# Kernel tuning notes

Hardware: AMD Instinct MI355X
Metric: run time of the kernel (lower is better)

## Reference

```python
import jax, jax.numpy as jnp
import numpy as np

EPS_LN = 1e-5

def _layernorm(x, g, b):
    mu = jnp.mean(x, axis=-1, keepdims=True)
    var = jnp.mean((x - mu) ** 2, axis=-1, keepdims=True)
    return (x - mu) * jax.lax.rsqrt(var + EPS_LN) * g + b

def _act_quant_ste(x):
    # clip_val uses detached stats -> stop_gradient
    clip_val = jax.lax.stop_gradient(
        jnp.clip(jnp.mean(jnp.abs(x), axis=-1, keepdims=True), 1e-8, None)) * 2.5
    scale = clip_val / 127.0
    x_scaled = x / scale
    x_clip = jnp.clip(x_scaled, -127.0, 127.0)
    x_q = x_scaled + jax.lax.stop_gradient(jnp.round(x_clip) - x_scaled)
    return x_q * scale

def _weight_quant_ste(w):
    scale = jax.lax.stop_gradient(jnp.clip(jnp.mean(jnp.abs(w)), 1e-8, None))
    w_norm = w / scale
    w_clip = jnp.clip(w_norm, -1.0, 1.0)
    w_q = w_norm + jax.lax.stop_gradient(jnp.round(w_clip) - w_norm)
    return w_q * scale

def _bitlinear(x, w, g, b):
    # w: [out, in]; x: [B,T,in]
    x_q = _act_quant_ste(_layernorm(x, g, b))
    w_q = _weight_quant_ste(w)
    return jnp.einsum('btd,hd->bth', x_q, w_q)

def setup_inputs() -> dict:
    D, H = 2048, 2048 * 4
    B, T = 4, 2048
    key = jax.random.key(0)
    ks = jax.random.split(key, 4)
    std = 0.02
    return {
        'x': jax.random.normal(ks[0], (B, T, D), dtype=jnp.float32),
        'mu_k': jnp.zeros((1, 1, D), jnp.float32),
        'mu_r': jnp.zeros((1, 1, D), jnp.float32),
        'wk': jax.random.normal(ks[1], (H, D), jnp.float32) * std,
        'gk': jnp.ones((D,), jnp.float32), 'bk': jnp.zeros((D,), jnp.float32),
        'wr': jax.random.normal(ks[2], (D, D), jnp.float32) * std,
        'gr': jnp.ones((D,), jnp.float32), 'br': jnp.zeros((D,), jnp.float32),
        'wv': jax.random.normal(ks[3], (D, H), jnp.float32) * std,
        'gv': jnp.ones((H,), jnp.float32), 'bv': jnp.zeros((H,), jnp.float32),
    }

def reference(x, mu_k, mu_r, wk, gk, bk, wr, gr, br, wv, gv, bv):
    B, T, C = x.shape
    prev = jnp.zeros((B, 1, C), dtype=x.dtype)  # state=None path
    x_prev = jnp.concatenate([prev, x[:, :-1, :]], axis=1)  # token shift
    dx = x_prev - x
    k_act = jax.nn.relu(_bitlinear(x + dx * mu_k, wk, gk, bk)) ** 2  # [B,T,H]
    rgate = jax.nn.sigmoid(_bitlinear(x + dx * mu_r, wr, gr, br))    # [B,T,D]
    out = rgate * _bitlinear(k_act, wv, gv, bv)                      # [B,T,D]
    return out, jax.lax.stop_gradient(x[:, -1:, :])
```

## Files before the change

### kernel.cpp

```cpp
#include <hip/hip_runtime.h>

#define T_LEN 2048
#define B_SZ  4
#define D_DIM 2048
#define H_DIM 8192
#define BT    (B_SZ * T_LEN)

typedef float f32x4 __attribute__((ext_vector_type(4)));
typedef int   i32x4v __attribute__((ext_vector_type(4)));
typedef int   i32x16v __attribute__((ext_vector_type(16)));
typedef unsigned short ushort8 __attribute__((ext_vector_type(8)));

__device__ __forceinline__ float bf2f(unsigned short u) {
    unsigned int i = ((unsigned int)u) << 16;
    return __builtin_bit_cast(float, i);
}
__device__ __forceinline__ unsigned short f2bf(float f) {
    unsigned int i = __builtin_bit_cast(unsigned int, f);
    i += 0x7fffu + ((i >> 16) & 1u);
    return (unsigned short)(i >> 16);
}

__device__ __forceinline__ float block_sum(float v, float* red) {
    #pragma unroll
    for (int o = 32; o > 0; o >>= 1) v += __shfl_down(v, o, 64);
    const int lane = threadIdx.x & 63, w = threadIdx.x >> 6;
    if (lane == 0) red[w] = v;
    __syncthreads();
    float r = red[0] + red[1] + red[2] + red[3];
    __syncthreads();
    return r;
}

__global__ void wabs_all(const float* __restrict__ wk, const float* __restrict__ wr,
                         const float* __restrict__ wv, float* __restrict__ part) {
    __shared__ float red[16];
    const int m = blockIdx.x >> 10;
    const int blk = blockIdx.x & 1023;
    const float* w = (m == 0) ? wk : (m == 1) ? wr : wv;
    const int n = (m == 1) ? D_DIM * D_DIM : H_DIM * D_DIM;
    float s = 0.f;
    int i = (blk * 256 + threadIdx.x) * 8;
    const int stride = 1024 * 256 * 8;
    for (; i < n; i += stride) {
        f32x4 a = *(const f32x4*)(w + i);
        f32x4 b = *(const f32x4*)(w + i + 4);
        #pragma unroll
        for (int j = 0; j < 4; j++) s += fabsf(a[j]) + fabsf(b[j]);
    }
    float tot = block_sum(s, red);
    if (threadIdx.x == 0) part[blockIdx.x] = tot;
}

__global__ void wfinal_all(const float* __restrict__ part, float* __restrict__ wsc) {
    __shared__ float red[16];
    const int m = blockIdx.x;
    const int n = (m == 1) ? D_DIM * D_DIM : H_DIM * D_DIM;
    float s = 0.f;
    for (int i = threadIdx.x; i < 1024; i += 256) s += part[m * 1024 + i];
    float tot = block_sum(s, red);
    if (threadIdx.x == 0) wsc[m] = fmaxf(tot / (float)n, 1e-8f);
}

__global__ void wquant_all(const float* __restrict__ wk, const float* __restrict__ wr,
                           const float* __restrict__ wv,
                           signed char* __restrict__ qk, signed char* __restrict__ qr,
                           signed char* __restrict__ qv,
                           const float* __restrict__ wsc) {
    const int b = blockIdx.x;
    int m, blk, nblk;
    if (b < 2048)      { m = 0; blk = b;        nblk = 2048; }
    else if (b < 3072) { m = 1; blk = b - 2048; nblk = 1024; }
    else               { m = 2; blk = b - 3072; nblk = 2048; }
    const float* w = (m == 0) ? wk : (m == 1) ? wr : wv;
    signed char* q = (m == 0) ? qk : (m == 1) ? qr : qv;
    const int n = (m == 1) ? D_DIM * D_DIM : H_DIM * D_DIM;
    const float s = wsc[m];
    int i = (blk * 256 + threadIdx.x) * 16;
    const int stride = nblk * 256 * 16;
    for (; i < n; i += stride) {
        union { signed char c[16]; i32x4v v; } pk;
        #pragma unroll
        for (int h = 0; h < 4; h++) {
            f32x4 a = *(const f32x4*)(w + i + h * 4);
            #pragma unroll
            for (int j = 0; j < 4; j++)
                pk.c[h * 4 + j] =
                    (signed char)(int)rintf(fminf(fmaxf(a[j] / s, -1.f), 1.f));
        }
        *(i32x4v*)(q + i) = pk.v;
    }
}

__device__ __forceinline__ void ln_quant8(const float* xm_in,
                                          const float* __restrict__ g,
                                          const float* __restrict__ b,
                                          signed char* qrow, float* srow, float* red) {
    const int base = threadIdx.x * 8;
    float xm[8];
    float s = 0.f;
    #pragma unroll
    for (int j = 0; j < 8; j++) { xm[j] = xm_in[j]; s += xm[j]; }
    const float mean = block_sum(s, red) * (1.f / D_DIM);
    float s2 = 0.f;
    #pragma unroll
    for (int j = 0; j < 8; j++) { float d = xm[j] - mean; s2 += d * d; }
    const float var  = block_sum(s2, red) * (1.f / D_DIM);
    const float rstd = 1.f / sqrtf(var + 1e-5f);
    f32x4 ga = *(const f32x4*)(g + base), gb = *(const f32x4*)(g + base + 4);
    f32x4 ba = *(const f32x4*)(b + base), bb2 = *(const f32x4*)(b + base + 4);
    float gg[8] = {ga[0],ga[1],ga[2],ga[3],gb[0],gb[1],gb[2],gb[3]};
    float bb[8] = {ba[0],ba[1],ba[2],ba[3],bb2[0],bb2[1],bb2[2],bb2[3]};
    float sa = 0.f;
    #pragma unroll
    for (int j = 0; j < 8; j++) {
        xm[j] = (xm[j] - mean) * rstd * gg[j] + bb[j];
        sa += fabsf(xm[j]);
    }
    const float amean = block_sum(sa, red) * (1.f / D_DIM);
    const float scale = fmaxf(amean, 1e-8f) * 2.5f / 127.0f;
    union { signed char c[8]; int2 v; } pk;
    #pragma unroll
    for (int j = 0; j < 8; j++)
        pk.c[j] = (signed char)(int)rintf(fminf(fmaxf(xm[j] / scale, -127.f), 127.f));
    *(int2*)(qrow + base) = pk.v;
    if (threadIdx.x == 0) *srow = scale;
}

__global__ void act_prep(const float* __restrict__ x,
                         const float* __restrict__ muk,
                         const float* __restrict__ gk, const float* __restrict__ bk,
                         const float* __restrict__ mur,
                         const float* __restrict__ gr, const float* __restrict__ br,
                         signed char* __restrict__ qk, float* __restrict__ sk,
                         signed char* __restrict__ qr, float* __restrict__ sr,
                         float* __restrict__ out2) {
    __shared__ float red[16];
    const int row = blockIdx.x;
    const int t = row & (T_LEN - 1);
    const int base = threadIdx.x * 8;

    float xv[8], xp[8];
    f32x4 xa = *(const f32x4*)(x + (size_t)row * D_DIM + base);
    f32x4 xb = *(const f32x4*)(x + (size_t)row * D_DIM + base + 4);
    xv[0]=xa[0]; xv[1]=xa[1]; xv[2]=xa[2]; xv[3]=xa[3];
    xv[4]=xb[0]; xv[5]=xb[1]; xv[6]=xb[2]; xv[7]=xb[3];
    if (t > 0) {
        f32x4 pa = *(const f32x4*)(x + (size_t)(row - 1) * D_DIM + base);
        f32x4 pb = *(const f32x4*)(x + (size_t)(row - 1) * D_DIM + base + 4);
        xp[0]=pa[0]; xp[1]=pa[1]; xp[2]=pa[2]; xp[3]=pa[3];
        xp[4]=pb[0]; xp[5]=pb[1]; xp[6]=pb[2]; xp[7]=pb[3];
    } else {
        #pragma unroll
        for (int j = 0; j < 8; j++) xp[j] = 0.f;
    }
    if (t == T_LEN - 1) {
        const int bb = row / T_LEN;
        *(f32x4*)(out2 + (size_t)bb * D_DIM + base)     = xa;
        *(f32x4*)(out2 + (size_t)bb * D_DIM + base + 4) = xb;
    }
    float mk[8], mr[8], xmk[8], xmr[8];
    f32x4 mka = *(const f32x4*)(muk + base), mkb = *(const f32x4*)(muk + base + 4);
    f32x4 mra = *(const f32x4*)(mur + base), mrb = *(const f32x4*)(mur + base + 4);
    mk[0]=mka[0]; mk[1]=mka[1]; mk[2]=mka[2]; mk[3]=mka[3];
    mk[4]=mkb[0]; mk[5]=mkb[1]; mk[6]=mkb[2]; mk[7]=mkb[3];
    mr[0]=mra[0]; mr[1]=mra[1]; mr[2]=mra[2]; mr[3]=mra[3];
    mr[4]=mrb[0]; mr[5]=mrb[1]; mr[6]=mrb[2]; mr[7]=mrb[3];
    #pragma unroll
    for (int j = 0; j < 8; j++) {
        const float dx = xp[j] - xv[j];
        xmk[j] = xv[j] + dx * mk[j];
        xmr[j] = xv[j] + dx * mr[j];
    }
    ln_quant8(xmk, gk, bk, qk + (size_t)row * D_DIM, sk + row, red);
    ln_quant8(xmr, gr, br, qr + (size_t)row * D_DIM, sr + row, red);
}

__global__ void lnq_v(const unsigned short* __restrict__ kact,
                      const float* __restrict__ g, const float* __restrict__ b,
                      signed char* __restrict__ qv, float* __restrict__ sv) {
    __shared__ float red[16];
    const int row = blockIdx.x;
    const int base = threadIdx.x * 32;
    const unsigned short* kr = kact + (size_t)row * H_DIM + base;

    float v[32];
    float s = 0.f;
    #pragma unroll
    for (int c = 0; c < 4; c++) {
        ushort8 a = *(const ushort8*)(kr + c * 8);
        #pragma unroll
        for (int j = 0; j < 8; j++) { v[c * 8 + j] = bf2f(a[j]); s += v[c * 8 + j]; }
    }
    const float mean = block_sum(s, red) * (1.f / H_DIM);
    float s2 = 0.f;
    #pragma unroll
    for (int j = 0; j < 32; j++) { float d = v[j] - mean; s2 += d * d; }
    const float var  = block_sum(s2, red) * (1.f / H_DIM);
    const float rstd = 1.f / sqrtf(var + 1e-5f);
    float sa = 0.f;
    #pragma unroll
    for (int c = 0; c < 8; c++) {
        f32x4 ga = *(const f32x4*)(g + base + c * 4);
        f32x4 ba = *(const f32x4*)(b + base + c * 4);
        #pragma unroll
        for (int j = 0; j < 4; j++) {
            int k = c * 4 + j;
            v[k] = (v[k] - mean) * rstd * ga[j] + ba[j];
            sa += fabsf(v[k]);
        }
    }
    const float amean = block_sum(sa, red) * (1.f / H_DIM);
    const float scale = fmaxf(amean, 1e-8f) * 2.5f / 127.0f;
    union { signed char c[32]; i32x4v v4[2]; } pk;
    #pragma unroll
    for (int j = 0; j < 32; j++)
        pk.c[j] = (signed char)(int)rintf(fminf(fmaxf(v[j] / scale, -127.f), 127.f));
    *(i32x4v*)(qv + (size_t)row * H_DIM + base)      = pk.v4[0];
    *(i32x4v*)(qv + (size_t)row * H_DIM + base + 16) = pk.v4[1];
    if (threadIdx.x == 0) sv[row] = scale;
}

__global__ __launch_bounds__(512, 2) void gemmA(
    const signed char* __restrict__ A, const signed char* __restrict__ B,
    int K, int Nn, int gn,
    const float* __restrict__ sa, const float* __restrict__ swp,
    unsigned short* __restrict__ out_bf) {
    __shared__ signed char Bs[2][128 * 64];
    const int tid = threadIdx.x;
    const int nwg = gridDim.x, q8 = nwg >> 3;
    const int swz = (blockIdx.x & 7) * q8 + (blockIdx.x >> 3);
    const int bm = swz / gn, bn = swz % gn;
    const int lane = tid & 63, wave = tid >> 6;
    const int lrow = lane & 31, lhalf = lane >> 5;
    const size_t arow0 = (size_t)bm * 512;
    const size_t brow0 = (size_t)bn * 128;
    const int NT = K >> 6;

    i32x16v acc[2][4] = {};

    auto stageB = [&](int buf, int k0) {
        const int r = tid >> 2, sl = tid & 3;
        const signed char* g = B + (brow0 + r) * (size_t)K + k0 + ((sl ^ ((r >> 1) & 3)) * 16);
        __builtin_amdgcn_global_load_lds(
            (const __attribute__((address_space(1))) void*)g,
            (__attribute__((address_space(3))) void*)(Bs[buf] + tid * 16), 16, 0, 0);
    };
    auto loadA = [&](i32x4v (&a)[2][2], int k0) {
        #pragma unroll
        for (int tm = 0; tm < 2; tm++)
            #pragma unroll
            for (int s = 0; s < 2; s++) {
                const int r = wave * 64 + tm * 32 + lrow;
                a[tm][s] = *(const i32x4v*)(A + (arow0 + r) * (size_t)K + k0 + (s * 2 + lhalf) * 16);
            }
    };
    auto readB = [&](const signed char* BsB, i32x4v (&b)[4][2]) {
        #pragma unroll
        for (int s = 0; s < 2; s++) {
            const int slot = s * 2 + lhalf;
            #pragma unroll
            for (int tn = 0; tn < 4; tn++) {
                const int r = tn * 32 + lrow;
                b[tn][s] = *(const i32x4v*)(BsB + r * 64 + ((slot ^ ((r >> 1) & 3)) * 16));
            }
        }
    };
    auto mfma8 = [&](i32x4v (&a)[2][2], i32x4v (&b)[4][2]) {
        #pragma unroll
        for (int s = 0; s < 2; s++)
            #pragma unroll
            for (int tm = 0; tm < 2; tm++)
                #pragma unroll
                for (int tn = 0; tn < 4; tn++)
                    acc[tm][tn] = __builtin_amdgcn_mfma_i32_32x32x32_i8(
                        a[tm][s], b[tn][s], acc[tm][tn], 0, 0, 0);
    };

    i32x4v a0[2][2], a1[2][2];
    stageB(0, 0);
    loadA(a0, 0);
    for (int it = 0; it < NT / 2; it++) {
        const int t0 = 2 * it, t1 = t0 + 1;
        stageB(1, t1 << 6);
        loadA(a1, t1 << 6);
        asm volatile("s_waitcnt vmcnt(5)" ::: "memory");
        __builtin_amdgcn_sched_barrier(0);
        __builtin_amdgcn_s_barrier();
        __builtin_amdgcn_sched_barrier(0);
        {
            i32x4v b[4][2];
            readB(Bs[0], b);
            __builtin_amdgcn_s_setprio(1);
            mfma8(a0, b);
            __builtin_amdgcn_s_setprio(0);
        }
        __builtin_amdgcn_sched_barrier(0);
        __builtin_amdgcn_s_barrier();
        if (t1 + 1 < NT) {
            stageB(0, (t1 + 1) << 6);
            loadA(a0, (t1 + 1) << 6);
            asm volatile("s_waitcnt vmcnt(5)" ::: "memory");
        } else {
            asm volatile("s_waitcnt vmcnt(0)" ::: "memory");
        }
        __builtin_amdgcn_sched_barrier(0);
        __builtin_amdgcn_s_barrier();
        __builtin_amdgcn_sched_barrier(0);
        {
            i32x4v b[4][2];
            readB(Bs[1], b);
            __builtin_amdgcn_s_setprio(1);
            mfma8(a1, b);
            __builtin_amdgcn_s_setprio(0);
        }
        __builtin_amdgcn_sched_barrier(0);
        __builtin_amdgcn_s_barrier();
    }

    const float sw = *swp;
    #pragma unroll
    for (int tm = 0; tm < 2; tm++) {
        #pragma unroll
        for (int tn = 0; tn < 4; tn++) {
            #pragma unroll
            for (int rg = 0; rg < 16; rg++) {
                const int rin  = (rg & 3) + 8 * (rg >> 2) + 4 * lhalf;
                const int grow = bm * 512 + wave * 64 + tm * 32 + rin;
                const int gcol = bn * 128 + tn * 32 + lrow;
                const float v = (float)acc[tm][tn][rg] * sa[grow] * sw;
                float rv = fmaxf(v, 0.f);
                out_bf[(size_t)grow * Nn + gcol] = f2bf(rv * rv);
            }
        }
    }
}

template <int EP>
__global__ __launch_bounds__(256) void gemm_i8(
    const signed char* __restrict__ A, const signed char* __restrict__ B,
    int K, int Nn,
    const float* __restrict__ sa, const float* __restrict__ swp,
    const unsigned short* __restrict__ gate_bf, float* __restrict__ out_f,
    unsigned short* __restrict__ out_gbf) {
    __shared__ signed char As[128 * 128];
    __shared__ signed char Bs[128 * 128];
    const int tid  = threadIdx.x;
    const int bm   = blockIdx.x, bn = blockIdx.y;
    const int lane = tid & 63, wave = tid >> 6;
    const int wr = wave >> 1, wc = wave & 1;
    const int lrow = lane & 31, lhalf = lane >> 5;

    i32x16v acc[2][2] = {};

    int srow[4], scol[4];
    #pragma unroll
    for (int i = 0; i < 4; i++) {
        int o = i * 256 + tid;
        int r = o >> 3, sl = o & 7;
        srow[i] = r;
        scol[i] = ((sl ^ (r & 7)) * 16);
    }
    const size_t arow0 = (size_t)bm * 128;
    const size_t brow0 = (size_t)bn * 128;

    for (int k0 = 0; k0 < K; k0 += 128) {
        __syncthreads();
        #pragma unroll
        for (int i = 0; i < 4; i++) {
            const signed char* ga = A + (arow0 + srow[i]) * (size_t)K + k0 + scol[i];
            const signed char* gb = B + (brow0 + srow[i]) * (size_t)K + k0 + scol[i];
            __builtin_amdgcn_global_load_lds(
                (const __attribute__((address_space(1))) void*)ga,
                (__attribute__((address_space(3))) void*)(As + (i * 256 + tid) * 16),
                16, 0, 0);
            __builtin_amdgcn_global_load_lds(
                (const __attribute__((address_space(1))) void*)gb,
                (__attribute__((address_space(3))) void*)(Bs + (i * 256 + tid) * 16),
                16, 0, 0);
        }
        __syncthreads();

        #pragma unroll
        for (int ks = 0; ks < 4; ks++) {
            const int slot = ks * 2 + lhalf;
            i32x4v af[2], bfv[2];
            #pragma unroll
            for (int tm = 0; tm < 2; tm++) {
                int r = wr * 64 + tm * 32 + lrow;
                af[tm] = *(const i32x4v*)(As + r * 128 + ((slot ^ (r & 7)) * 16));
            }
            #pragma unroll
            for (int tn = 0; tn < 2; tn++) {
                int r = wc * 64 + tn * 32 + lrow;
                bfv[tn] = *(const i32x4v*)(Bs + r * 128 + ((slot ^ (r & 7)) * 16));
            }
            #pragma unroll
            for (int tm = 0; tm < 2; tm++)
                #pragma unroll
                for (int tn = 0; tn < 2; tn++)
                    acc[tm][tn] = __builtin_amdgcn_mfma_i32_32x32x32_i8(
                        af[tm], bfv[tn], acc[tm][tn], 0, 0, 0);
        }
    }

    const float sw = *swp;
    #pragma unroll
    for (int tm = 0; tm < 2; tm++) {
        #pragma unroll
        for (int tn = 0; tn < 2; tn++) {
            #pragma unroll
            for (int rg = 0; rg < 16; rg++) {
                const int rin  = (rg & 3) + 8 * (rg >> 2) + 4 * lhalf;
                const int grow = bm * 128 + wr * 64 + tm * 32 + rin;
                const int gcol = bn * 128 + wc * 64 + tn * 32 + lrow;
                const float v = (float)acc[tm][tn][rg] * sa[grow] * sw;
                const size_t idx = (size_t)grow * Nn + gcol;
                if (EP == 1) {
                    out_gbf[idx] = f2bf(1.0f / (1.0f + expf(-v)));
                } else {
                    out_f[idx] = bf2f(gate_bf[idx]) * v;
                }
            }
        }
    }
}

extern "C" void kernel_launch(void* const* d_in, const int* in_sizes, int n_in,
                              void* d_out, int out_size, void* d_ws, size_t ws_size,
                              hipStream_t stream) {
    const float* x   = (const float*)d_in[0];
    const float* muk = (const float*)d_in[1];
    const float* mur = (const float*)d_in[2];
    const float* wk  = (const float*)d_in[3];
    const float* gk  = (const float*)d_in[4];
    const float* bk  = (const float*)d_in[5];
    const float* wr  = (const float*)d_in[6];
    const float* gr  = (const float*)d_in[7];
    const float* br  = (const float*)d_in[8];
    const float* wv  = (const float*)d_in[9];
    const float* gv  = (const float*)d_in[10];
    const float* bv  = (const float*)d_in[11];

    char* wsb = (char*)d_ws;
    size_t off = 0;
    auto alloc = [&](size_t bytes) -> size_t {
        size_t p = off;
        off = (off + bytes + 255) & ~(size_t)255;
        return p;
    };
    const size_t o_wqk  = alloc((size_t)H_DIM * D_DIM);
    const size_t o_wqr  = alloc((size_t)D_DIM * D_DIM);
    const size_t o_wqv  = alloc((size_t)D_DIM * H_DIM);
    const size_t o_wsc  = alloc(64);
    const size_t o_part = alloc(3 * 1024 * sizeof(float));
    const size_t o_xqk  = alloc((size_t)BT * D_DIM);
    const size_t o_xqr  = alloc((size_t)BT * D_DIM);
    const size_t o_gate = alloc((size_t)BT * D_DIM * 2);
    const size_t o_sk   = alloc((size_t)BT * 4);
    const size_t o_sr   = alloc((size_t)BT * 4);
    const size_t fixed  = off;

    int CH = BT;
    while (CH > 512 &&
           fixed + (size_t)CH * (H_DIM + 2 * H_DIM + 4) + 8192 > ws_size)
        CH >>= 1;
    const size_t o_xqv  = alloc((size_t)CH * H_DIM);
    const size_t o_kact = alloc((size_t)CH * H_DIM * 2);
    const size_t o_sv   = alloc((size_t)CH * 4);

    signed char* wqk = (signed char*)(wsb + o_wqk);
    signed char* wqr = (signed char*)(wsb + o_wqr);
    signed char* wqv = (signed char*)(wsb + o_wqv);
    float* wsc  = (float*)(wsb + o_wsc);
    float* part = (float*)(wsb + o_part);
    signed char* xqk = (signed char*)(wsb + o_xqk);
    signed char* xqr = (signed char*)(wsb + o_xqr);
    unsigned short* gate = (unsigned short*)(wsb + o_gate);
    float* sk = (float*)(wsb + o_sk);
    float* sr = (float*)(wsb + o_sr);
    signed char* xqv = (signed char*)(wsb + o_xqv);
    unsigned short* kact = (unsigned short*)(wsb + o_kact);
    float* sv = (float*)(wsb + o_sv);

    float* outp = (float*)d_out;
    float* out2 = outp + (size_t)BT * D_DIM;

    wabs_all<<<3072, 256, 0, stream>>>(wk, wr, wv, part);
    wfinal_all<<<3, 256, 0, stream>>>(part, wsc);
    wquant_all<<<5120, 256, 0, stream>>>(wk, wr, wv, wqk, wqr, wqv, wsc);

    act_prep<<<BT, 256, 0, stream>>>(x, muk, gk, bk, mur, gr, br,
                                     xqk, sk, xqr, sr, out2);

    gemm_i8<1><<<dim3(BT / 128, D_DIM / 128), 256, 0, stream>>>(
        xqr, wqr, D_DIM, D_DIM, sr, wsc + 1,
        (const unsigned short*)nullptr, (float*)nullptr, gate);

    for (int row0 = 0; row0 < BT; row0 += CH) {
        gemmA<<<(CH / 512) * (H_DIM / 128), 512, 0, stream>>>(
            xqk + (size_t)row0 * D_DIM, wqk, D_DIM, H_DIM, H_DIM / 128,
            sk + row0, wsc + 0, kact);

        lnq_v<<<CH, 256, 0, stream>>>(kact, gv, bv, xqv, sv);

        gemm_i8<2><<<dim3(CH / 128, D_DIM / 128), 256, 0, stream>>>(
            xqv, wqv, H_DIM, D_DIM, sv, wsc + 2,
            gate + (size_t)row0 * D_DIM, outp + (size_t)row0 * D_DIM,
            (unsigned short*)nullptr);
    }
}
```

Before: 652.7 us.

## Unify int8 GEMMs into templated register-A kernel with 4-stage B pipeline

Replaces the separate 128x128 LDS-staged gemm_i8 kernel with a templated version of the register-A, LDS-B GEMM. It now runs with 256-row tiles for the r-gate and v projections and 512-row tiles for the k projection. The B buffer grows to four LDS stages with a prefetch distance of two, which leaves one barrier per k-step instead of two. The aim is better latency hiding and less synchronisation on all three GEMMs. In exchange it uses more LDS and larger tiles, which means fewer workgroups for the D-output GEMMs.

```diff
diff --git a/kernel.cpp b/kernel.cpp
--- a/kernel.cpp
+++ b/kernel.cpp
@@ -221,23 +221,26 @@
     if (threadIdx.x == 0) sv[row] = scale;
 }
 
-__global__ __launch_bounds__(512, 2) void gemmA(
+template <int EP, int MT>
+__global__ __launch_bounds__(512, 2) void gemmR(
     const signed char* __restrict__ A, const signed char* __restrict__ B,
     int K, int Nn, int gn,
     const float* __restrict__ sa, const float* __restrict__ swp,
+    const unsigned short* __restrict__ gate_bf, float* __restrict__ out_f,
     unsigned short* __restrict__ out_bf) {
-    __shared__ signed char Bs[2][128 * 64];
+    constexpr int BM = MT * 256;
+    __shared__ signed char Bs[4][128 * 64];
     const int tid = threadIdx.x;
     const int nwg = gridDim.x, q8 = nwg >> 3;
     const int swz = (blockIdx.x & 7) * q8 + (blockIdx.x >> 3);
     const int bm = swz / gn, bn = swz % gn;
     const int lane = tid & 63, wave = tid >> 6;
     const int lrow = lane & 31, lhalf = lane >> 5;
-    const size_t arow0 = (size_t)bm * 512;
+    const size_t arow0 = (size_t)bm * BM;
     const size_t brow0 = (size_t)bn * 128;
     const int NT = K >> 6;
 
-    i32x16v acc[2][4] = {};
+    i32x16v acc[MT][4] = {};
 
     auto stageB = [&](int buf, int k0) {
         const int r = tid >> 2, sl = tid & 3;
@@ -246,12 +249,12 @@
             (const __attribute__((address_space(1))) void*)g,
             (__attribute__((address_space(3))) void*)(Bs[buf] + tid * 16), 16, 0, 0);
     };
-    auto loadA = [&](i32x4v (&a)[2][2], int k0) {
-        #pragma unroll
-        for (int tm = 0; tm < 2; tm++)
+    auto loadA = [&](i32x4v (&a)[MT][2], int k0) {
+        #pragma unroll
+        for (int tm = 0; tm < MT; tm++)
             #pragma unroll
             for (int s = 0; s < 2; s++) {
-                const int r = wave * 64 + tm * 32 + lrow;
+                const int r = wave * (MT * 32) + tm * 32 + lrow;
                 a[tm][s] = *(const i32x4v*)(A + (arow0 + r) * (size_t)K + k0 + (s * 2 + lhalf) * 16);
             }
     };
@@ -266,158 +269,69 @@
             }
         }
     };
-    auto mfma8 = [&](i32x4v (&a)[2][2], i32x4v (&b)[4][2]) {
+    auto mfmaT = [&](i32x4v (&a)[MT][2], i32x4v (&b)[4][2]) {
         #pragma unroll
         for (int s = 0; s < 2; s++)
             #pragma unroll
-            for (int tm = 0; tm < 2; tm++)
+            for (int tm = 0; tm < MT; tm++)
                 #pragma unroll
                 for (int tn = 0; tn < 4; tn++)
                     acc[tm][tn] = __builtin_amdgcn_mfma_i32_32x32x32_i8(
                         a[tm][s], b[tn][s], acc[tm][tn], 0, 0, 0);
     };
 
-    i32x4v a0[2][2], a1[2][2];
+    i32x4v aE[MT][2], aO[MT][2];
     stageB(0, 0);
-    loadA(a0, 0);
-    for (int it = 0; it < NT / 2; it++) {
-        const int t0 = 2 * it, t1 = t0 + 1;
-        stageB(1, t1 << 6);
-        loadA(a1, t1 << 6);
-        asm volatile("s_waitcnt vmcnt(5)" ::: "memory");
+    loadA(aE, 0);
+    stageB(1, 64);
+
+    auto body = [&](int t, i32x4v (&cur)[MT][2], i32x4v (&nxt)[MT][2]) {
+        const bool hasA = (t + 1 < NT);
+        const bool hasB = (t + 2 < NT);
+        if (hasA) loadA(nxt, (t + 1) << 6);
+        if (hasB) stageB((t + 2) & 3, (t + 2) << 6);
+        if (hasB) {
+            if constexpr (MT == 2) asm volatile("s_waitcnt vmcnt(6)" ::: "memory");
+            else                   asm volatile("s_waitcnt vmcnt(4)" ::: "memory");
+        } else if (hasA) {
+            if constexpr (MT == 2) asm volatile("s_waitcnt vmcnt(5)" ::: "memory");
+            else                   asm volatile("s_waitcnt vmcnt(3)" ::: "memory");
+        } else {
+            asm volatile("s_waitcnt vmcnt(0)" ::: "memory");
+        }
         __builtin_amdgcn_sched_barrier(0);
         __builtin_amdgcn_s_barrier();
-        __builtin_amdgcn_sched_barrier(0);
         {
             i32x4v b[4][2];
-            readB(Bs[0], b);
+            readB(Bs[t & 3], b);
             __builtin_amdgcn_s_setprio(1);
-            mfma8(a0, b);
+            mfmaT(cur, b);
             __builtin_amdgcn_s_setprio(0);
         }
-        __builtin_amdgcn_sched_barrier(0);
-        __builtin_amdgcn_s_barrier();
-        if (t1 + 1 < NT) {
-            stageB(0, (t1 + 1) << 6);
-            loadA(a0, (t1 + 1) << 6);
-            asm volatile("s_waitcnt vmcnt(5)" ::: "memory");
-        } else {
-            asm volatile("s_waitcnt vmcnt(0)" ::: "memory");
-        }
-        __builtin_amdgcn_sched_barrier(0);
-        __builtin_amdgcn_s_barrier();
-        __builtin_amdgcn_sched_barrier(0);
-        {
-            i32x4v b[4][2];
-            readB(Bs[1], b);
-            __builtin_amdgcn_s_setprio(1);
-            mfma8(a1, b);
-            __builtin_amdgcn_s_setprio(0);
-        }
-        __builtin_amdgcn_sched_barrier(0);
-        __builtin_amdgcn_s_barrier();
+    };
+
+    for (int t = 0; t < NT; t += 2) {
+        body(t, aE, aO);
+        body(t + 1, aO, aE);
     }
 
     const float sw = *swp;
     #pragma unroll
-    for (int tm = 0; tm < 2; tm++) {
+    for (int tm = 0; tm < MT; tm++) {
         #pragma unroll
         for (int tn = 0; tn < 4; tn++) {
             #pragma unroll
             for (int rg = 0; rg < 16; rg++) {
                 const int rin  = (rg & 3) + 8 * (rg >> 2) + 4 * lhalf;
-                const int grow = bm * 512 + wave * 64 + tm * 32 + rin;
+                const int grow = bm * BM + wave * (MT * 32) + tm * 32 + rin;
                 const int gcol = bn * 128 + tn * 32 + lrow;
                 const float v = (float)acc[tm][tn][rg] * sa[grow] * sw;
-                float rv = fmaxf(v, 0.f);
-                out_bf[(size_t)grow * Nn + gcol] = f2bf(rv * rv);
-            }
-        }
-    }
-}
-
-template <int EP>
-__global__ __launch_bounds__(256) void gemm_i8(
-    const signed char* __restrict__ A, const signed char* __restrict__ B,
-    int K, int Nn,
-    const float* __restrict__ sa, const float* __restrict__ swp,
-    const unsigned short* __restrict__ gate_bf, float* __restrict__ out_f,
-    unsigned short* __restrict__ out_gbf) {
-    __shared__ signed char As[128 * 128];
-    __shared__ signed char Bs[128 * 128];
-    const int tid  = threadIdx.x;
-    const int bm   = blockIdx.x, bn = blockIdx.y;
-    const int lane = tid & 63, wave = tid >> 6;
-    const int wr = wave >> 1, wc = wave & 1;
-    const int lrow = lane & 31, lhalf = lane >> 5;
-
-    i32x16v acc[2][2] = {};
-
-    int srow[4], scol[4];
-    #pragma unroll
-    for (int i = 0; i < 4; i++) {
-        int o = i * 256 + tid;
-        int r = o >> 3, sl = o & 7;
-        srow[i] = r;
-        scol[i] = ((sl ^ (r & 7)) * 16);
-    }
-    const size_t arow0 = (size_t)bm * 128;
-    const size_t brow0 = (size_t)bn * 128;
-
-    for (int k0 = 0; k0 < K; k0 += 128) {
-        __syncthreads();
-        #pragma unroll
-        for (int i = 0; i < 4; i++) {
-            const signed char* ga = A + (arow0 + srow[i]) * (size_t)K + k0 + scol[i];
-            const signed char* gb = B + (brow0 + srow[i]) * (size_t)K + k0 + scol[i];
-            __builtin_amdgcn_global_load_lds(
-                (const __attribute__((address_space(1))) void*)ga,
-                (__attribute__((address_space(3))) void*)(As + (i * 256 + tid) * 16),
-                16, 0, 0);
-            __builtin_amdgcn_global_load_lds(
-                (const __attribute__((address_space(1))) void*)gb,
-                (__attribute__((address_space(3))) void*)(Bs + (i * 256 + tid) * 16),
-                16, 0, 0);
-        }
-        __syncthreads();
-
-        #pragma unroll
-        for (int ks = 0; ks < 4; ks++) {
-            const int slot = ks * 2 + lhalf;
-            i32x4v af[2], bfv[2];
-            #pragma unroll
-            for (int tm = 0; tm < 2; tm++) {
-                int r = wr * 64 + tm * 32 + lrow;
-                af[tm] = *(const i32x4v*)(As + r * 128 + ((slot ^ (r & 7)) * 16));
-            }
-            #pragma unroll
-            for (int tn = 0; tn < 2; tn++) {
-                int r = wc * 64 + tn * 32 + lrow;
-                bfv[tn] = *(const i32x4v*)(Bs + r * 128 + ((slot ^ (r & 7)) * 16));
-            }
-            #pragma unroll
-            for (int tm = 0; tm < 2; tm++)
-                #pragma unroll
-                for (int tn = 0; tn < 2; tn++)
-                    acc[tm][tn] = __builtin_amdgcn_mfma_i32_32x32x32_i8(
-                        af[tm], bfv[tn], acc[tm][tn], 0, 0, 0);
-        }
-    }
-
-    const float sw = *swp;
-    #pragma unroll
-    for (int tm = 0; tm < 2; tm++) {
-        #pragma unroll
-        for (int tn = 0; tn < 2; tn++) {
-            #pragma unroll
-            for (int rg = 0; rg < 16; rg++) {
-                const int rin  = (rg & 3) + 8 * (rg >> 2) + 4 * lhalf;
-                const int grow = bm * 128 + wr * 64 + tm * 32 + rin;
-                const int gcol = bn * 128 + wc * 64 + tn * 32 + lrow;
-                const float v = (float)acc[tm][tn][rg] * sa[grow] * sw;
                 const size_t idx = (size_t)grow * Nn + gcol;
-                if (EP == 1) {
-                    out_gbf[idx] = f2bf(1.0f / (1.0f + expf(-v)));
+                if (EP == 0) {
+                    float rv = fmaxf(v, 0.f);
+                    out_bf[idx] = f2bf(rv * rv);
+                } else if (EP == 1) {
+                    out_bf[idx] = f2bf(1.0f / (1.0f + expf(-v)));
                 } else {
                     out_f[idx] = bf2f(gate_bf[idx]) * v;
                 }
@@ -493,19 +407,20 @@
     act_prep<<<BT, 256, 0, stream>>>(x, muk, gk, bk, mur, gr, br,
                                      xqk, sk, xqr, sr, out2);
 
-    gemm_i8<1><<<dim3(BT / 128, D_DIM / 128), 256, 0, stream>>>(
-        xqr, wqr, D_DIM, D_DIM, sr, wsc + 1,
+    gemmR<1, 1><<<(BT / 256) * (D_DIM / 128), 512, 0, stream>>>(
+        xqr, wqr, D_DIM, D_DIM, D_DIM / 128, sr, wsc + 1,
         (const unsigned short*)nullptr, (float*)nullptr, gate);
 
     for (int row0 = 0; row0 < BT; row0 += CH) {
-        gemmA<<<(CH / 512) * (H_DIM / 128), 512, 0, stream>>>(
+        gemmR<0, 2><<<(CH / 512) * (H_DIM / 128), 512, 0, stream>>>(
             xqk + (size_t)row0 * D_DIM, wqk, D_DIM, H_DIM, H_DIM / 128,
-            sk + row0, wsc + 0, kact);
+            sk + row0, wsc + 0,
+            (const unsigned short*)nullptr, (float*)nullptr, kact);
 
         lnq_v<<<CH, 256, 0, stream>>>(kact, gv, bv, xqv, sv);
 
-        gemm_i8<2><<<dim3(CH / 128, D_DIM / 128), 256, 0, stream>>>(
-            xqv, wqv, H_DIM, D_DIM, sv, wsc + 2,
+        gemmR<2, 1><<<(CH / 256) * (D_DIM / 128), 512, 0, stream>>>(
+            xqv, wqv, H_DIM, D_DIM, D_DIM / 128, sv, wsc + 2,
             gate + (size_t)row0 * D_DIM, outp + (size_t)row0 * D_DIM,
             (unsigned short*)nullptr);
     }
```

Result: slower. 674.0 us (+3.3%).
